# Kernel tuning notes

Measured on AMD Instinct MI355X. Metric: run time of the kernel, lower is better.

Reference implementation:

```python
import jax, jax.numpy as jnp
import numpy as np

N_NODES = 20000
N_EDGES = 160000
IN_DIM = 512
HID = 256
N_CLASSES = 2
NUM_GRAPHS = 16


def setup_inputs() -> dict:
    key = jax.random.key(0)
    ks = jax.random.split(key, 12)
    x = jax.random.normal(ks[0], (N_NODES, IN_DIM), dtype=jnp.float32)
    edge_index = jax.random.randint(ks[1], (2, N_EDGES), 0, N_NODES, dtype=jnp.int64)
    batch = jnp.sort(jax.random.randint(ks[2], (N_NODES,), 0, NUM_GRAPHS, dtype=jnp.int64))
    def glorot(k, shape):
        lim = float(np.sqrt(6.0 / (shape[0] + shape[1])))
        return jax.random.uniform(k, shape, jnp.float32, -lim, lim)
    return {
        "x": x,
        "edge_index": edge_index,
        "batch": batch,
        "W1n": glorot(ks[3], (IN_DIM, HID)),
        "W1s": glorot(ks[4], (IN_DIM, HID)),
        "b1": jnp.zeros((HID,), jnp.float32),
        "W2n": glorot(ks[5], (HID, HID)),
        "W2s": glorot(ks[6], (HID, HID)),
        "b2": jnp.zeros((HID,), jnp.float32),
        "fc1w": glorot(ks[7], (HID, HID // 2)),
        "fc1b": jnp.zeros((HID // 2,), jnp.float32),
        "fc2w": glorot(ks[8], (HID // 2, N_CLASSES)),
        "fc2b": jnp.zeros((N_CLASSES,), jnp.float32),
    }


def _sage_conv(x, W_nbr, W_self, b, src, dst, n_nodes):
    # mean-aggregate neighbor features (messages flow src -> dst, PyG convention)
    deg = jax.ops.segment_sum(jnp.ones(src.shape, x.dtype), dst, num_segments=n_nodes)
    deg = jnp.maximum(deg, 1.0)
    aggr = jax.ops.segment_sum(x[src], dst, num_segments=n_nodes) / deg[:, None]
    # SAGEConv: lin_l(aggr) + lin_r(x) + bias (equivalent to concat-linear)
    return aggr @ W_nbr + x @ W_self + b


def reference(x, edge_index, batch, W1n, W1s, b1, W2n, W2s, b2, fc1w, fc1b, fc2w, fc2b):
    src, dst = edge_index[0], edge_index[1]
    n = x.shape[0]
    h = jax.nn.relu(_sage_conv(x, W1n, W1s, b1, src, dst, n))
    h = jax.nn.relu(_sage_conv(h, W2n, W2s, b2, src, dst, n))
    # global_mean_pool over graph ids
    cnt = jax.ops.segment_sum(jnp.ones((n,), h.dtype), batch, num_segments=NUM_GRAPHS)
    pooled = jax.ops.segment_sum(h, batch, num_segments=NUM_GRAPHS) / jnp.maximum(cnt, 1.0)[:, None]
    out = jax.nn.relu(pooled @ fc1w + fc1b) @ fc2w + fc2b
    return out
```

## Files before the change

### kernel.cpp

```cpp
#include <hip/hip_runtime.h>
#include <hip/hip_bf16.h>


#define HID 256
#define NCOL 512

typedef __bf16 bf16x8 __attribute__((ext_vector_type(8)));
typedef float floatx4 __attribute__((ext_vector_type(4)));
typedef unsigned int u32;
typedef const u32 __attribute__((address_space(1)))* gp_t;
typedef u32 __attribute__((address_space(3)))* lp_t;

__device__ __forceinline__ ushort f2bf(float f) {
    unsigned u = __float_as_uint(f);
    u += 0x7fffu + ((u >> 16) & 1u);
    return (ushort)(u >> 16);
}
__device__ __forceinline__ float bf2f(ushort b) {
    return __uint_as_float(((unsigned)b) << 16);
}

__device__ __forceinline__ void packT_work(const float* __restrict__ Wn,
                                           const float* __restrict__ Ws,
                                           ushort* __restrict__ WT, int K, int gid) {
    if (gid >= NCOL * K) return;
    int n = gid / K, k = gid - n * K;
    float v = (n < HID) ? Wn[k * HID + n] : Ws[k * HID + (n - HID)];
    WT[gid] = f2bf(v);
}

__global__ void prep_kernel(const float* __restrict__ x, ushort* __restrict__ xb, int n4,
                            const float* __restrict__ W1n, const float* __restrict__ W1s,
                            ushort* __restrict__ w1t, int K1,
                            const float* __restrict__ W2n, const float* __restrict__ W2s,
                            ushort* __restrict__ w2t, int K2,
                            const int* __restrict__ dst, int* __restrict__ degi, int n_edges,
                            int nb_cvt, int nb_w1, int nb_w2) {
    int bx = blockIdx.x, t = threadIdx.x;
    if (bx < nb_cvt) {
        int i = bx * 256 + t;
        if (i < n4) {
            float4 v = ((const float4*)x)[i];
            ushort4 o;
            o.x = f2bf(v.x); o.y = f2bf(v.y); o.z = f2bf(v.z); o.w = f2bf(v.w);
            ((ushort4*)xb)[i] = o;
        }
    } else if (bx < nb_cvt + nb_w1) {
        packT_work(W1n, W1s, w1t, K1, (bx - nb_cvt) * 256 + t);
    } else if (bx < nb_cvt + nb_w1 + nb_w2) {
        packT_work(W2n, W2s, w2t, K2, (bx - nb_cvt - nb_w1) * 256 + t);
    } else {
        int e = (bx - nb_cvt - nb_w1 - nb_w2) * 256 + t;
        if (e < n_edges) atomicAdd(&degi[dst[e]], 1);
    }
}

__global__ __launch_bounds__(256) void psum_kernel(const int* __restrict__ degi,
                                                   int* __restrict__ partials, int n) {
    int t = threadIdx.x;
    int i = blockIdx.x * 256 + t;
    int v = (i < n) ? degi[i] : 0;
#pragma unroll
    for (int d = 1; d < 64; d <<= 1) v += __shfl_xor(v, d, 64);
    __shared__ int wsum[4];
    if ((t & 63) == 0) wsum[t >> 6] = v;
    __syncthreads();
    if (t == 0) partials[blockIdx.x] = wsum[0] + wsum[1] + wsum[2] + wsum[3];
}

__global__ __launch_bounds__(64) void pscan_kernel(int* __restrict__ partials,
                                                   int* __restrict__ off, int nb, int n) {
    int lane = threadIdx.x;
    int carry = 0;
    for (int base = 0; base < nb; base += 256) {
        int i0 = base + lane * 4;
        int v0 = (i0 + 0 < nb) ? partials[i0 + 0] : 0;
        int v1 = (i0 + 1 < nb) ? partials[i0 + 1] : 0;
        int v2 = (i0 + 2 < nb) ? partials[i0 + 2] : 0;
        int v3 = (i0 + 3 < nb) ? partials[i0 + 3] : 0;
        int local = v0 + v1 + v2 + v3;
        int s = local;
#pragma unroll
        for (int d = 1; d < 64; d <<= 1) {
            int t = __shfl_up(s, d, 64);
            if (lane >= d) s += t;
        }
        int excl = carry + s - local;
        if (i0 + 0 < nb) partials[i0 + 0] = excl;
        excl += v0;
        if (i0 + 1 < nb) partials[i0 + 1] = excl;
        excl += v1;
        if (i0 + 2 < nb) partials[i0 + 2] = excl;
        excl += v2;
        if (i0 + 3 < nb) partials[i0 + 3] = excl;
        carry += __shfl(s, 63, 64);
    }
    if (lane == 0) off[n] = carry;
}

__global__ __launch_bounds__(256) void scan2_kernel(const int* __restrict__ degi,
                                                    const int* __restrict__ partials,
                                                    int* __restrict__ off,
                                                    int* __restrict__ cursor, int n) {
    int t = threadIdx.x, lane = t & 63, w = t >> 6;
    int i = blockIdx.x * 256 + t;
    int v = (i < n) ? degi[i] : 0;
    int s = v;
#pragma unroll
    for (int d = 1; d < 64; d <<= 1) {
        int u = __shfl_up(s, d, 64);
        if (lane >= d) s += u;
    }
    __shared__ int wsum[4];
    if (lane == 63) wsum[w] = s;
    __syncthreads();
    int woff = 0;
    for (int k = 0; k < w; ++k) woff += wsum[k];
    int excl = partials[blockIdx.x] + woff + s - v;
    if (i < n) { off[i] = excl; cursor[i] = excl; }
}

__global__ void fill_kernel(const int* __restrict__ src, const int* __restrict__ dst,
                            int* __restrict__ cursor, int* __restrict__ eidx, int n_edges) {
    int e = blockIdx.x * 256 + threadIdx.x;
    if (e < n_edges) {
        int p = atomicAdd(&cursor[dst[e]], 1);
        eidx[p] = src[e];
    }
}

__global__ __launch_bounds__(256) void gemm_mfma(const ushort* __restrict__ A,
                                                 const ushort* __restrict__ BT,
                                                 ushort* __restrict__ Y, int K, int nG) {
    int b = blockIdx.x;
    int xcd = b & 7, rest = b >> 3;
    int m = rest & 3, Ggrp = rest >> 2;
    int G = xcd + 8 * Ggrp;
    if (G >= nG) return;
    int m0 = G * 64, n0 = m * 128;

    __shared__ ushort As[2][64 * 64];
    __shared__ ushort Bs[2][128 * 64];
    int tid = threadIdx.x;
    int w = tid >> 6, lane = tid & 63;
    int quad = lane >> 4, r16 = lane & 15;
    int wm = (w >> 1) * 32, wn = (w & 1) * 64;

    int arow[2], agu[2], brow[4], bgu[4];
#pragma unroll
    for (int rr = 0; rr < 2; ++rr) {
        int idx = rr * 256 + tid;
        arow[rr] = idx >> 3;
        agu[rr] = (idx & 7) ^ (arow[rr] & 7);
    }
#pragma unroll
    for (int rr = 0; rr < 4; ++rr) {
        int idx = rr * 256 + tid;
        brow[rr] = idx >> 3;
        bgu[rr] = (idx & 7) ^ (brow[rr] & 7);
    }

    auto stage = [&](int buf, int k0) {
#pragma unroll
        for (int rr = 0; rr < 2; ++rr) {
            const ushort* ga = A + (size_t)(m0 + arow[rr]) * K + k0 + agu[rr] * 8;
            ushort* la = As[buf] + (size_t)(rr * 256 + w * 64) * 8;
            __builtin_amdgcn_global_load_lds((gp_t)(const void*)ga, (lp_t)(void*)la, 16, 0, 0);
        }
#pragma unroll
        for (int rr = 0; rr < 4; ++rr) {
            const ushort* gb = BT + (size_t)(n0 + brow[rr]) * K + k0 + bgu[rr] * 8;
            ushort* lb = Bs[buf] + (size_t)(rr * 256 + w * 64) * 8;
            __builtin_amdgcn_global_load_lds((gp_t)(const void*)gb, (lp_t)(void*)lb, 16, 0, 0);
        }
    };

    floatx4 acc[2][4];
#pragma unroll
    for (int i = 0; i < 2; ++i)
#pragma unroll
        for (int j = 0; j < 4; ++j) acc[i][j] = (floatx4){0.f, 0.f, 0.f, 0.f};

    const int nk = K >> 6;
    stage(0, 0);
    for (int t = 0; t < nk; ++t) {
        int cb = t & 1;
        __syncthreads();
        if (t + 1 < nk) stage(cb ^ 1, (t + 1) << 6);
        const ushort* Ab = As[cb];
        const ushort* Bb = Bs[cb];
#pragma unroll
        for (int s = 0; s < 2; ++s) {
            bf16x8 a[2], b2[4];
#pragma unroll
            for (int i = 0; i < 2; ++i) {
                int row = wm + i * 16 + r16;
                int au = (s * 4 + quad) ^ (row & 7);
                a[i] = *(const bf16x8*)(Ab + row * 64 + au * 8);
            }
#pragma unroll
            for (int j = 0; j < 4; ++j) {
                int row = wn + j * 16 + r16;
                int bu = (s * 4 + quad) ^ (row & 7);
                b2[j] = *(const bf16x8*)(Bb + row * 64 + bu * 8);
            }
#pragma unroll
            for (int i = 0; i < 2; ++i)
#pragma unroll
                for (int j = 0; j < 4; ++j)
                    acc[i][j] = __builtin_amdgcn_mfma_f32_16x16x32_bf16(a[i], b2[j], acc[i][j], 0, 0, 0);
        }
    }
#pragma unroll
    for (int i = 0; i < 2; ++i)
#pragma unroll
        for (int j = 0; j < 4; ++j) {
            int col = n0 + wn + j * 16 + r16;
#pragma unroll
            for (int rg = 0; rg < 4; ++rg) {
                int row = m0 + wm + i * 16 + quad * 4 + rg;
                Y[(size_t)row * NCOL + col] = f2bf(acc[i][j][rg]);
            }
        }
}

__global__ __launch_bounds__(256) void gather_kernel(const ushort* __restrict__ Y,
                                                     const int* __restrict__ off,
                                                     const int* __restrict__ eidx,
                                                     const float* __restrict__ bias,
                                                     ushort* __restrict__ h, int n_nodes) {
    int tid = threadIdx.x;
    int v = blockIdx.x * 4 + (tid >> 6);
    if (v >= n_nodes) return;
    int q4 = (tid & 63) << 2;
    int e0 = off[v], e1 = off[v + 1];
    ushort4 sv = *(const ushort4*)(Y + (size_t)v * NCOL + HID + q4);
    float4 b = *(const float4*)(bias + q4);
    float4 a0 = make_float4(0.f, 0.f, 0.f, 0.f), a1 = a0, a2 = a0, a3 = a0;
    int e = e0;
    for (; e + 3 < e1; e += 4) {
        int s0 = eidx[e], s1 = eidx[e + 1], s2 = eidx[e + 2], s3 = eidx[e + 3];
        ushort4 y0 = *(const ushort4*)(Y + (size_t)s0 * NCOL + q4);
        ushort4 y1 = *(const ushort4*)(Y + (size_t)s1 * NCOL + q4);
        ushort4 y2 = *(const ushort4*)(Y + (size_t)s2 * NCOL + q4);
        ushort4 y3 = *(const ushort4*)(Y + (size_t)s3 * NCOL + q4);
        a0.x += bf2f(y0.x); a0.y += bf2f(y0.y); a0.z += bf2f(y0.z); a0.w += bf2f(y0.w);
        a1.x += bf2f(y1.x); a1.y += bf2f(y1.y); a1.z += bf2f(y1.z); a1.w += bf2f(y1.w);
        a2.x += bf2f(y2.x); a2.y += bf2f(y2.y); a2.z += bf2f(y2.z); a2.w += bf2f(y2.w);
        a3.x += bf2f(y3.x); a3.y += bf2f(y3.y); a3.z += bf2f(y3.z); a3.w += bf2f(y3.w);
    }
    for (; e < e1; ++e) {
        ushort4 y = *(const ushort4*)(Y + (size_t)eidx[e] * NCOL + q4);
        a0.x += bf2f(y.x); a0.y += bf2f(y.y); a0.z += bf2f(y.z); a0.w += bf2f(y.w);
    }
    float invd = 1.0f / fmaxf((float)(e1 - e0), 1.0f);
    ushort4 r;
    r.x = f2bf(fmaxf((a0.x + a1.x + a2.x + a3.x) * invd + bf2f(sv.x) + b.x, 0.f));
    r.y = f2bf(fmaxf((a0.y + a1.y + a2.y + a3.y) * invd + bf2f(sv.y) + b.y, 0.f));
    r.z = f2bf(fmaxf((a0.z + a1.z + a2.z + a3.z) * invd + bf2f(sv.z) + b.z, 0.f));
    r.w = f2bf(fmaxf((a0.w + a1.w + a2.w + a3.w) * invd + bf2f(sv.w) + b.w, 0.f));
    *(ushort4*)(h + (size_t)v * HID + q4) = r;
}

__global__ void pool_kernel(const ushort* __restrict__ h, const int* __restrict__ batch,
                            float* __restrict__ pooled, float* __restrict__ cnt, int n_nodes) {
    int f = threadIdx.x;
    int v0 = blockIdx.x * 64;
    int vend = min(v0 + 64, n_nodes);
    if (v0 >= n_nodes) return;
    int cur = batch[v0];
    float acc = 0.f, ac = 0.f;
    for (int v = v0; v < vend; ++v) {
        int g = batch[v];
        if (g != cur) {
            atomicAdd(&pooled[cur * HID + f], acc);
            if (f == 0) atomicAdd(&cnt[cur], ac);
            acc = 0.f; ac = 0.f; cur = g;
        }
        acc += bf2f(h[(size_t)v * HID + f]);
        ac += 1.0f;
    }
    atomicAdd(&pooled[cur * HID + f], acc);
    if (f == 0) atomicAdd(&cnt[cur], ac);
}

__global__ void head_kernel(const float* __restrict__ pooled, const float* __restrict__ cnt,
                            const float* __restrict__ fc1w, const float* __restrict__ fc1b,
                            const float* __restrict__ fc2w, const float* __restrict__ fc2b,
                            float* __restrict__ out) {
    int g = blockIdx.x, j = threadIdx.x;
    __shared__ float p[256];
    __shared__ float hid[128];
    float inv = 1.0f / fmaxf(cnt[g], 1.0f);
    p[j] = pooled[g * HID + j] * inv;
    p[j + 128] = pooled[g * HID + 128 + j] * inv;
    __syncthreads();
    float a = fc1b[j];
    for (int f = 0; f < 256; ++f) a += p[f] * fc1w[f * 128 + j];
    hid[j] = fmaxf(a, 0.f);
    __syncthreads();
    if (j < 2) {
        float o = fc2b[j];
        for (int t = 0; t < 128; ++t) o += hid[t] * fc2w[t * 2 + j];
        out[g * 2 + j] = o;
    }
}

extern "C" void kernel_launch(void* const* d_in, const int* in_sizes, int n_in,
                              void* d_out, int out_size, void* d_ws, size_t ws_size,
                              hipStream_t stream) {
    const float* x    = (const float*)d_in[0];
    const int*   ei   = (const int*)d_in[1];
    const int*   batch= (const int*)d_in[2];
    const float* W1n  = (const float*)d_in[3];
    const float* W1s  = (const float*)d_in[4];
    const float* b1   = (const float*)d_in[5];
    const float* W2n  = (const float*)d_in[6];
    const float* W2s  = (const float*)d_in[7];
    const float* b2   = (const float*)d_in[8];
    const float* fc1w = (const float*)d_in[9];
    const float* fc1b = (const float*)d_in[10];
    const float* fc2w = (const float*)d_in[11];
    const float* fc2b = (const float*)d_in[12];
    float* out = (float*)d_out;

    const int n_nodes = in_sizes[2];
    const int n_edges = in_sizes[1] / 2;
    const int in_dim  = in_sizes[0] / n_nodes;
    const int Mpad    = (n_nodes + 63) & ~63;
    const int nb      = (n_nodes + 255) / 256;
    const int nG      = Mpad / 64;
    const int* src = ei;
    const int* dst = ei + n_edges;

    char* wsb = (char*)d_ws;
    size_t cur = 0;
    auto alloc = [&](size_t nbytes) { size_t o = cur; cur = (cur + nbytes + 255) & ~(size_t)255; return o; };
    size_t o_degi = alloc((size_t)n_nodes * 4);
    size_t o_off  = alloc((size_t)(n_nodes + 1) * 4);
    size_t o_cur  = alloc((size_t)n_nodes * 4);
    size_t o_part = alloc((size_t)nb * 4);
    size_t o_eidx = alloc((size_t)n_edges * 4);
    size_t o_w1   = alloc((size_t)NCOL * in_dim * 2);
    size_t o_w2   = alloc((size_t)NCOL * HID * 2);
    size_t o_xb   = alloc((size_t)Mpad * in_dim * 2);
    size_t o_hb   = alloc((size_t)Mpad * HID * 2);
    size_t o_y    = alloc((size_t)Mpad * NCOL * 2);
    size_t o_pool = alloc((size_t)16 * HID * 4 + 16 * 4);
    (void)ws_size;

    int*    degi    = (int*)(wsb + o_degi);
    int*    off     = (int*)(wsb + o_off);
    int*    cursor  = (int*)(wsb + o_cur);
    int*    partials= (int*)(wsb + o_part);
    int*    eidx    = (int*)(wsb + o_eidx);
    ushort* w1t     = (ushort*)(wsb + o_w1);
    ushort* w2t     = (ushort*)(wsb + o_w2);
    ushort* xb      = (ushort*)(wsb + o_xb);
    ushort* hb      = (ushort*)(wsb + o_hb);
    ushort* Y       = (ushort*)(wsb + o_y);
    float*  pooled  = (float*)(wsb + o_pool);
    float*  cnt     = pooled + 16 * HID;

    hipMemsetAsync(degi, 0, (size_t)n_nodes * 4, stream);
    hipMemsetAsync(pooled, 0, (size_t)(16 * HID + 16) * 4, stream);

    int n4 = n_nodes * in_dim / 4;
    int nb_cvt = (n4 + 255) / 256;
    int nb_w1  = (NCOL * in_dim + 255) / 256;
    int nb_w2  = (NCOL * HID + 255) / 256;
    int nb_deg = (n_edges + 255) / 256;
    prep_kernel<<<nb_cvt + nb_w1 + nb_w2 + nb_deg, 256, 0, stream>>>(
        x, xb, n4, W1n, W1s, w1t, in_dim, W2n, W2s, w2t, HID,
        dst, degi, n_edges, nb_cvt, nb_w1, nb_w2);

    psum_kernel<<<nb, 256, 0, stream>>>(degi, partials, n_nodes);
    pscan_kernel<<<1, 64, 0, stream>>>(partials, off, nb, n_nodes);
    scan2_kernel<<<nb, 256, 0, stream>>>(degi, partials, off, cursor, n_nodes);
    fill_kernel<<<(n_edges + 255) / 256, 256, 0, stream>>>(src, dst, cursor, eidx, n_edges);

    int gemm_blocks = 8 * 4 * ((nG + 7) / 8);
    int gather_blocks = (n_nodes + 3) / 4;

    gemm_mfma<<<gemm_blocks, 256, 0, stream>>>(xb, w1t, Y, in_dim, nG);
    gather_kernel<<<gather_blocks, 256, 0, stream>>>(Y, off, eidx, b1, hb, n_nodes);

    gemm_mfma<<<gemm_blocks, 256, 0, stream>>>(hb, w2t, Y, HID, nG);
    gather_kernel<<<gather_blocks, 256, 0, stream>>>(Y, off, eidx, b2, hb, n_nodes);

    pool_kernel<<<(n_nodes + 63) / 64, 256, 0, stream>>>(hb, batch, pooled, cnt, n_nodes);
    head_kernel<<<16, 128, 0, stream>>>(pooled, cnt, fc1w, fc1b, fc2w, fc2b, out);
}
```

Baseline: 229.7 us.

## Fuse scan passes, load edge indices by lane shuffle, merge pool and head

Drops the single-block pscan kernel: each scan2 block now sums the partials ahead of it by itself and block 0 writes the total. The gather kernel loads up to 64 edge indices with one coalesced read and broadcasts them by shuffle, with an 8-way unroll, instead of each lane reading eidx separately. Pooling and the MLP head are merged into one 16-block kernel that finds each graph's node range by binary search on the sorted batch array, which removes the atomics and the pooled memset. The risk is that the tail now runs on only 16 blocks, each reading its graph's ~1250 nodes serially, which may be slower than the many-block atomic pooling it replaces.

```diff
diff --git a/kernel.cpp b/kernel.cpp
--- a/kernel.cpp
+++ b/kernel.cpp
@@ -68,42 +68,26 @@
     if (t == 0) partials[blockIdx.x] = wsum[0] + wsum[1] + wsum[2] + wsum[3];
 }
 
-__global__ __launch_bounds__(64) void pscan_kernel(int* __restrict__ partials,
-                                                   int* __restrict__ off, int nb, int n) {
-    int lane = threadIdx.x;
-    int carry = 0;
-    for (int base = 0; base < nb; base += 256) {
-        int i0 = base + lane * 4;
-        int v0 = (i0 + 0 < nb) ? partials[i0 + 0] : 0;
-        int v1 = (i0 + 1 < nb) ? partials[i0 + 1] : 0;
-        int v2 = (i0 + 2 < nb) ? partials[i0 + 2] : 0;
-        int v3 = (i0 + 3 < nb) ? partials[i0 + 3] : 0;
-        int local = v0 + v1 + v2 + v3;
-        int s = local;
-#pragma unroll
-        for (int d = 1; d < 64; d <<= 1) {
-            int t = __shfl_up(s, d, 64);
-            if (lane >= d) s += t;
-        }
-        int excl = carry + s - local;
-        if (i0 + 0 < nb) partials[i0 + 0] = excl;
-        excl += v0;
-        if (i0 + 1 < nb) partials[i0 + 1] = excl;
-        excl += v1;
-        if (i0 + 2 < nb) partials[i0 + 2] = excl;
-        excl += v2;
-        if (i0 + 3 < nb) partials[i0 + 3] = excl;
-        carry += __shfl(s, 63, 64);
-    }
-    if (lane == 0) off[n] = carry;
-}
-
 __global__ __launch_bounds__(256) void scan2_kernel(const int* __restrict__ degi,
                                                     const int* __restrict__ partials,
                                                     int* __restrict__ off,
-                                                    int* __restrict__ cursor, int n) {
+                                                    int* __restrict__ cursor, int n, int nb) {
     int t = threadIdx.x, lane = t & 63, w = t >> 6;
-    int i = blockIdx.x * 256 + t;
+    int c = blockIdx.x;
+    int pre = 0, tot = 0;
+    for (int base = 0; base < nb; base += 64) {
+        int idx = base + lane;
+        int pv = (idx < nb) ? partials[idx] : 0;
+        pre += (idx < c) ? pv : 0;
+        tot += pv;
+    }
+#pragma unroll
+    for (int d = 1; d < 64; d <<= 1) {
+        pre += __shfl_xor(pre, d, 64);
+        tot += __shfl_xor(tot, d, 64);
+    }
+    if (c == 0 && t == 0) off[n] = tot;
+    int i = c * 256 + t;
     int v = (i < n) ? degi[i] : 0;
     int s = v;
 #pragma unroll
@@ -116,7 +100,7 @@
     __syncthreads();
     int woff = 0;
     for (int k = 0; k < w; ++k) woff += wsum[k];
-    int excl = partials[blockIdx.x] + woff + s - v;
+    int excl = pre + woff + s - v;
     if (i < n) { off[i] = excl; cursor[i] = excl; }
 }
 
@@ -224,6 +208,7 @@
         }
 }
 
+#define ACC4(A, Yv) { A.x += bf2f(Yv.x); A.y += bf2f(Yv.y); A.z += bf2f(Yv.z); A.w += bf2f(Yv.w); }
 __global__ __launch_bounds__(256) void gather_kernel(const ushort* __restrict__ Y,
                                                      const int* __restrict__ off,
                                                      const int* __restrict__ eidx,
@@ -232,26 +217,37 @@
     int tid = threadIdx.x;
     int v = blockIdx.x * 4 + (tid >> 6);
     if (v >= n_nodes) return;
-    int q4 = (tid & 63) << 2;
+    int lane = tid & 63;
+    int q4 = lane << 2;
     int e0 = off[v], e1 = off[v + 1];
     ushort4 sv = *(const ushort4*)(Y + (size_t)v * NCOL + HID + q4);
     float4 b = *(const float4*)(bias + q4);
     float4 a0 = make_float4(0.f, 0.f, 0.f, 0.f), a1 = a0, a2 = a0, a3 = a0;
-    int e = e0;
-    for (; e + 3 < e1; e += 4) {
-        int s0 = eidx[e], s1 = eidx[e + 1], s2 = eidx[e + 2], s3 = eidx[e + 3];
-        ushort4 y0 = *(const ushort4*)(Y + (size_t)s0 * NCOL + q4);
-        ushort4 y1 = *(const ushort4*)(Y + (size_t)s1 * NCOL + q4);
-        ushort4 y2 = *(const ushort4*)(Y + (size_t)s2 * NCOL + q4);
-        ushort4 y3 = *(const ushort4*)(Y + (size_t)s3 * NCOL + q4);
-        a0.x += bf2f(y0.x); a0.y += bf2f(y0.y); a0.z += bf2f(y0.z); a0.w += bf2f(y0.w);
-        a1.x += bf2f(y1.x); a1.y += bf2f(y1.y); a1.z += bf2f(y1.z); a1.w += bf2f(y1.w);
-        a2.x += bf2f(y2.x); a2.y += bf2f(y2.y); a2.z += bf2f(y2.z); a2.w += bf2f(y2.w);
-        a3.x += bf2f(y3.x); a3.y += bf2f(y3.y); a3.z += bf2f(y3.z); a3.w += bf2f(y3.w);
-    }
-    for (; e < e1; ++e) {
-        ushort4 y = *(const ushort4*)(Y + (size_t)eidx[e] * NCOL + q4);
-        a0.x += bf2f(y.x); a0.y += bf2f(y.y); a0.z += bf2f(y.z); a0.w += bf2f(y.w);
+    for (int base = e0; base < e1; base += 64) {
+        int ecnt = min(64, e1 - base);
+        int ev = (lane < ecnt) ? eidx[base + lane] : 0;
+        int j = 0;
+        for (; j + 8 <= ecnt; j += 8) {
+            int s0 = __shfl(ev, j + 0), s1 = __shfl(ev, j + 1);
+            int s2 = __shfl(ev, j + 2), s3 = __shfl(ev, j + 3);
+            int s4 = __shfl(ev, j + 4), s5 = __shfl(ev, j + 5);
+            int s6 = __shfl(ev, j + 6), s7 = __shfl(ev, j + 7);
+            ushort4 y0 = *(const ushort4*)(Y + (size_t)s0 * NCOL + q4);
+            ushort4 y1 = *(const ushort4*)(Y + (size_t)s1 * NCOL + q4);
+            ushort4 y2 = *(const ushort4*)(Y + (size_t)s2 * NCOL + q4);
+            ushort4 y3 = *(const ushort4*)(Y + (size_t)s3 * NCOL + q4);
+            ushort4 y4 = *(const ushort4*)(Y + (size_t)s4 * NCOL + q4);
+            ushort4 y5 = *(const ushort4*)(Y + (size_t)s5 * NCOL + q4);
+            ushort4 y6 = *(const ushort4*)(Y + (size_t)s6 * NCOL + q4);
+            ushort4 y7 = *(const ushort4*)(Y + (size_t)s7 * NCOL + q4);
+            ACC4(a0, y0); ACC4(a1, y1); ACC4(a2, y2); ACC4(a3, y3);
+            ACC4(a0, y4); ACC4(a1, y5); ACC4(a2, y6); ACC4(a3, y7);
+        }
+        for (; j < ecnt; ++j) {
+            int s = __shfl(ev, j);
+            ushort4 y = *(const ushort4*)(Y + (size_t)s * NCOL + q4);
+            ACC4(a0, y);
+        }
     }
     float invd = 1.0f / fmaxf((float)(e1 - e0), 1.0f);
     ushort4 r;
@@ -262,47 +258,44 @@
     *(ushort4*)(h + (size_t)v * HID + q4) = r;
 }
 
-__global__ void pool_kernel(const ushort* __restrict__ h, const int* __restrict__ batch,
-                            float* __restrict__ pooled, float* __restrict__ cnt, int n_nodes) {
-    int f = threadIdx.x;
-    int v0 = blockIdx.x * 64;
-    int vend = min(v0 + 64, n_nodes);
-    if (v0 >= n_nodes) return;
-    int cur = batch[v0];
-    float acc = 0.f, ac = 0.f;
-    for (int v = v0; v < vend; ++v) {
-        int g = batch[v];
-        if (g != cur) {
-            atomicAdd(&pooled[cur * HID + f], acc);
-            if (f == 0) atomicAdd(&cnt[cur], ac);
-            acc = 0.f; ac = 0.f; cur = g;
-        }
-        acc += bf2f(h[(size_t)v * HID + f]);
-        ac += 1.0f;
-    }
-    atomicAdd(&pooled[cur * HID + f], acc);
-    if (f == 0) atomicAdd(&cnt[cur], ac);
-}
-
-__global__ void head_kernel(const float* __restrict__ pooled, const float* __restrict__ cnt,
-                            const float* __restrict__ fc1w, const float* __restrict__ fc1b,
-                            const float* __restrict__ fc2w, const float* __restrict__ fc2b,
-                            float* __restrict__ out) {
-    int g = blockIdx.x, j = threadIdx.x;
+__global__ __launch_bounds__(256) void tail_kernel(const ushort* __restrict__ h,
+                                                   const int* __restrict__ batch,
+                                                   const float* __restrict__ fc1w,
+                                                   const float* __restrict__ fc1b,
+                                                   const float* __restrict__ fc2w,
+                                                   const float* __restrict__ fc2b,
+                                                   float* __restrict__ out, int n_nodes) {
+    int g = blockIdx.x, t = threadIdx.x;
+    auto lb = [&](int key) {
+        int lo = 0, hi = n_nodes;
+        while (lo < hi) { int mid = (lo + hi) >> 1; if (batch[mid] < key) lo = mid + 1; else hi = mid; }
+        return lo;
+    };
+    int lo = lb(g), hi = lb(g + 1);
+    float c0 = 0.f, c1 = 0.f, c2 = 0.f, c3 = 0.f;
+    int v = lo;
+    for (; v + 3 < hi; v += 4) {
+        c0 += bf2f(h[(size_t)(v + 0) * HID + t]);
+        c1 += bf2f(h[(size_t)(v + 1) * HID + t]);
+        c2 += bf2f(h[(size_t)(v + 2) * HID + t]);
+        c3 += bf2f(h[(size_t)(v + 3) * HID + t]);
+    }
+    for (; v < hi; ++v) c0 += bf2f(h[(size_t)v * HID + t]);
     __shared__ float p[256];
-    __shared__ float hid[128];
-    float inv = 1.0f / fmaxf(cnt[g], 1.0f);
-    p[j] = pooled[g * HID + j] * inv;
-    p[j + 128] = pooled[g * HID + 128 + j] * inv;
+    __shared__ float hidv[128];
+    float inv = 1.0f / fmaxf((float)(hi - lo), 1.0f);
+    p[t] = (c0 + c1 + c2 + c3) * inv;
     __syncthreads();
-    float a = fc1b[j];
-    for (int f = 0; f < 256; ++f) a += p[f] * fc1w[f * 128 + j];
-    hid[j] = fmaxf(a, 0.f);
+    if (t < 128) {
+        float a = fc1b[t];
+        for (int f = 0; f < 256; ++f) a += p[f] * fc1w[f * 128 + t];
+        hidv[t] = fmaxf(a, 0.f);
+    }
     __syncthreads();
-    if (j < 2) {
-        float o = fc2b[j];
-        for (int t = 0; t < 128; ++t) o += hid[t] * fc2w[t * 2 + j];
-        out[g * 2 + j] = o;
+    if (t < 2) {
+        float o = fc2b[t];
+        for (int k = 0; k < 128; ++k) o += hidv[k] * fc2w[k * 2 + t];
+        out[g * 2 + t] = o;
     }
 }
 
@@ -346,7 +339,6 @@
     size_t o_xb   = alloc((size_t)Mpad * in_dim * 2);
     size_t o_hb   = alloc((size_t)Mpad * HID * 2);
     size_t o_y    = alloc((size_t)Mpad * NCOL * 2);
-    size_t o_pool = alloc((size_t)16 * HID * 4 + 16 * 4);
     (void)ws_size;
 
     int*    degi    = (int*)(wsb + o_degi);
@@ -359,11 +351,8 @@
     ushort* xb      = (ushort*)(wsb + o_xb);
     ushort* hb      = (ushort*)(wsb + o_hb);
     ushort* Y       = (ushort*)(wsb + o_y);
-    float*  pooled  = (float*)(wsb + o_pool);
-    float*  cnt     = pooled + 16 * HID;
 
     hipMemsetAsync(degi, 0, (size_t)n_nodes * 4, stream);
-    hipMemsetAsync(pooled, 0, (size_t)(16 * HID + 16) * 4, stream);
 
     int n4 = n_nodes * in_dim / 4;
     int nb_cvt = (n4 + 255) / 256;
@@ -375,8 +364,7 @@
         dst, degi, n_edges, nb_cvt, nb_w1, nb_w2);
 
     psum_kernel<<<nb, 256, 0, stream>>>(degi, partials, n_nodes);
-    pscan_kernel<<<1, 64, 0, stream>>>(partials, off, nb, n_nodes);
-    scan2_kernel<<<nb, 256, 0, stream>>>(degi, partials, off, cursor, n_nodes);
+    scan2_kernel<<<nb, 256, 0, stream>>>(degi, partials, off, cursor, n_nodes, nb);
     fill_kernel<<<(n_edges + 255) / 256, 256, 0, stream>>>(src, dst, cursor, eidx, n_edges);
 
     int gemm_blocks = 8 * 4 * ((nG + 7) / 8);
@@ -388,6 +376,5 @@
     gemm_mfma<<<gemm_blocks, 256, 0, stream>>>(hb, w2t, Y, HID, nG);
     gather_kernel<<<gather_blocks, 256, 0, stream>>>(Y, off, eidx, b2, hb, n_nodes);
 
-    pool_kernel<<<(n_nodes + 63) / 64, 256, 0, stream>>>(hb, batch, pooled, cnt, n_nodes);
-    head_kernel<<<16, 128, 0, stream>>>(pooled, cnt, fc1w, fc1b, fc2w, fc2b, out);
-}
+    tail_kernel<<<16, 256, 0, stream>>>(hb, batch, fc1w, fc1b, fc2w, fc2b, out, n_nodes);
+}
```

New measurement: 291.1 us. 26.7% more time.
